# Kernel tuning notes

Hardware: AMD Instinct MI355X
Metric: run time of the kernel (lower is better)

## Reference

```python
import jax, jax.numpy as jnp
import numpy as np

TAYLOR_ORDER = 16      # Taylor terms after scaling (||A_s|| <= 0.5 -> machine precision)
MAX_SQUARINGS = 16     # fixed upper bound on squaring steps (jit-friendly)


def batched_expm(A):
    """Vectorized scaling-and-squaring matrix exponential for A of shape [..., n, n].

    Replaces the original per-item torch.linalg.matrix_exp Python loop with one
    fused batched computation (same math: exp(Q*t)).
    """
    n = A.shape[-1]
    I = jnp.eye(n, dtype=A.dtype)
    # per-matrix infinity norm [...,]
    nrm = jnp.max(jnp.sum(jnp.abs(A), axis=-1), axis=-1)
    # number of squarings so that scaled norm <= 0.5
    s = jnp.clip(jnp.ceil(jnp.log2(jnp.maximum(nrm, 1e-30) / 0.5)), 0.0, float(MAX_SQUARINGS))
    As = A * jnp.exp2(-s)[..., None, None]
    # Taylor series: P = I + As + As^2/2! + ...
    P = jnp.broadcast_to(I, A.shape)
    term = P
    for k in range(1, TAYLOR_ORDER + 1):
        term = jnp.matmul(term, As) / k
        P = P + term
    # undo scaling: square s times (data-dependent count via masked squaring)
    s_b = s[..., None, None]
    for i in range(MAX_SQUARINGS):
        P = jnp.where(s_b > i, jnp.matmul(P, P), P)
    return P


def setup_inputs() -> dict:
    key = jax.random.key(0)
    k1, k2 = jax.random.split(key)
    rate_matrix = jax.random.normal(k1, (64, 32768, 4, 4), dtype=jnp.float32)
    time = jax.random.uniform(k2, (64,), dtype=jnp.float32)
    return {"rate_matrix": rate_matrix, "time": time}


def reference(rate_matrix, time):
    # Qt = rate_matrix[i, j] * time[i], batched over (batch, seq_len)
    Qt = rate_matrix * time[:, None, None, None]
    return batched_expm(Qt)  # [B, S, 4, 4] transition probability matrices
```

## Files before the change

kernel.cpp:

```cpp
#include <hip/hip_runtime.h>
#include <math.h>


constexpr int TAYLOR_N = 10;

__global__ void __launch_bounds__(256) expm4_kernel(
    const float* __restrict__ A,
    const float* __restrict__ tvec,
    float* __restrict__ out,
    int M, int S)
{
    const int m = blockIdx.x * 256 + threadIdx.x;
    if (m >= M) return;

    const float t = tvec[m / S];

    float a[16];
    const float4* Ap = reinterpret_cast<const float4*>(A) + (size_t)m * 4;
    #pragma unroll
    for (int i = 0; i < 4; ++i) {
        float4 v = Ap[i];
        a[4*i+0] = v.x * t;
        a[4*i+1] = v.y * t;
        a[4*i+2] = v.z * t;
        a[4*i+3] = v.w * t;
    }

    float nrm = 0.0f;
    #pragma unroll
    for (int i = 0; i < 4; ++i) {
        float rs = fabsf(a[4*i+0]) + fabsf(a[4*i+1])
                 + fabsf(a[4*i+2]) + fabsf(a[4*i+3]);
        nrm = fmaxf(nrm, rs);
    }

    float sf = ceilf(log2f(fmaxf(nrm, 1e-30f) * 2.0f));
    sf = fminf(fmaxf(sf, 0.0f), 16.0f);
    const int   si    = (int)sf;
    const float scale = exp2f(-sf);
    #pragma unroll
    for (int i = 0; i < 16; ++i) a[i] *= scale;

    float P[16], T[16];
    #pragma unroll
    for (int i = 0; i < 16; ++i) { T[i] = a[i]; P[i] = a[i]; }
    P[0] += 1.0f; P[5] += 1.0f; P[10] += 1.0f; P[15] += 1.0f;

    #pragma unroll
    for (int k = 2; k <= TAYLOR_N; ++k) {
        const float rk = 1.0f / (float)k;
        #pragma unroll
        for (int i = 0; i < 4; ++i) {
            const float t0 = T[4*i+0], t1 = T[4*i+1];
            const float t2 = T[4*i+2], t3 = T[4*i+3];
            #pragma unroll
            for (int j = 0; j < 4; ++j) {
                float v = t0*a[j] + t1*a[4+j] + t2*a[8+j] + t3*a[12+j];
                v *= rk;
                T[4*i+j] = v;
                P[4*i+j] += v;
            }
        }
    }

    for (int it = 0; it < si; ++it) {
        float Q[16];
        #pragma unroll
        for (int i = 0; i < 4; ++i) {
            const float p0 = P[4*i+0], p1 = P[4*i+1];
            const float p2 = P[4*i+2], p3 = P[4*i+3];
            #pragma unroll
            for (int j = 0; j < 4; ++j) {
                Q[4*i+j] = p0*P[j] + p1*P[4+j] + p2*P[8+j] + p3*P[12+j];
            }
        }
        #pragma unroll
        for (int i = 0; i < 16; ++i) P[i] = Q[i];
    }

    float4* Op = reinterpret_cast<float4*>(out) + (size_t)m * 4;
    #pragma unroll
    for (int i = 0; i < 4; ++i) {
        float4 v;
        v.x = P[4*i+0]; v.y = P[4*i+1]; v.z = P[4*i+2]; v.w = P[4*i+3];
        Op[i] = v;
    }
}

extern "C" void kernel_launch(void* const* d_in, const int* in_sizes, int n_in,
                              void* d_out, int out_size, void* d_ws, size_t ws_size,
                              hipStream_t stream) {
    const float* A    = (const float*)d_in[0];
    const float* tvec = (const float*)d_in[1];
    float* out        = (float*)d_out;

    const int B = in_sizes[1];
    const int M = in_sizes[0] / 16;
    const int S = M / B;

    const int threads = 256;
    const int blocks  = (M + threads - 1) / threads;
    expm4_kernel<<<blocks, threads, 0, stream>>>(A, tvec, out, M, S);
}
```

Baseline: 231.9 us.

## Rewrite expm kernel with Paterson-Stockmeyer, packed math, and prefetching grid-stride loop

Replaces the sequential degree-10 Taylor evaluation with a Paterson-Stockmeyer style scheme built from A^2 and A^3, using packed float2 FMAs. The log2/exp2 scaling is replaced by exponent bit manipulation. The kernel becomes a grid-stride loop that double-buffers input loads through inline-asm global loads with manual waitcnt, and writes results with inline-asm stores. The time index per block is precomputed to avoid integer division. Together these aim to cut ALU work and hide memory latency, at the cost of fragile inline asm and reliance on the exact shape divisibility.

```diff
diff --git a/kernel.cpp b/kernel.cpp
--- a/kernel.cpp
+++ b/kernel.cpp
@@ -2,89 +2,206 @@
 #include <math.h>
 
 
-constexpr int TAYLOR_N = 10;
-
-__global__ void __launch_bounds__(256) expm4_kernel(
+typedef float f4 __attribute__((ext_vector_type(4)));
+typedef float f2 __attribute__((ext_vector_type(2)));
+
+constexpr int TPB   = 256;
+constexpr int KITER = 8;
+
+#define PREF(r, ptr)                                                         \
+    asm volatile("global_load_dwordx4 %0, %4, off\n\t"                       \
+                 "global_load_dwordx4 %1, %4, off offset:16\n\t"             \
+                 "global_load_dwordx4 %2, %4, off offset:32\n\t"             \
+                 "global_load_dwordx4 %3, %4, off offset:48"                 \
+                 : "=&v"(r##0), "=&v"(r##1), "=&v"(r##2), "=&v"(r##3)        \
+                 : "v"((const void*)(ptr)))
+
+#define WAITBUF(r)                                                           \
+    asm volatile("s_waitcnt vmcnt(4)"                                        \
+                 : "+v"(r##0), "+v"(r##1), "+v"(r##2), "+v"(r##3))
+
+#define STORE4(ptr, o0, o1, o2, o3)                                          \
+    asm volatile("global_store_dwordx4 %0, %1, off\n\t"                      \
+                 "global_store_dwordx4 %0, %2, off offset:16\n\t"            \
+                 "global_store_dwordx4 %0, %3, off offset:32\n\t"            \
+                 "global_store_dwordx4 %0, %4, off offset:48"                 \
+                 :: "v"((void*)(ptr)), "v"(o0), "v"(o1), "v"(o2), "v"(o3)    \
+                 : "memory")
+
+__device__ __forceinline__ f2 sp(float s) { f2 v; v.x = s; v.y = s; return v; }
+
+__device__ __forceinline__ void mm4p(f2 D[4][2], const f2 X[4][2],
+                                     const f2 Y[4][2])
+{
+    #pragma unroll
+    for (int i = 0; i < 4; ++i) {
+        const float x0 = X[i][0].x, x1 = X[i][0].y;
+        const float x2 = X[i][1].x, x3 = X[i][1].y;
+        #pragma unroll
+        for (int p = 0; p < 2; ++p) {
+            f2 acc = sp(x0) * Y[0][p];
+            acc = sp(x1) * Y[1][p] + acc;
+            acc = sp(x2) * Y[2][p] + acc;
+            acc = sp(x3) * Y[3][p] + acc;
+            D[i][p] = acc;
+        }
+    }
+}
+
+__device__ __forceinline__ void expm4_one(f4 r0, f4 r1, f4 r2, f4 r3, float t,
+                                          f4& o0, f4& o1, f4& o2, f4& o3)
+{
+    float nrm = fmaxf(
+        fmaxf(fabsf(r0.x)+fabsf(r0.y)+fabsf(r0.z)+fabsf(r0.w),
+              fabsf(r1.x)+fabsf(r1.y)+fabsf(r1.z)+fabsf(r1.w)),
+        fmaxf(fabsf(r2.x)+fabsf(r2.y)+fabsf(r2.z)+fabsf(r2.w),
+              fabsf(r3.x)+fabsf(r3.y)+fabsf(r3.z)+fabsf(r3.w)));
+    nrm *= fabsf(t);
+
+    const float    x = fmaxf(nrm, 1e-30f) * 2.0f;
+    const unsigned u = __float_as_uint(x);
+    int si = (int)(u >> 23) - 127 + ((u & 0x7fffffu) != 0u);
+    si = si < 0 ? 0 : (si > 16 ? 16 : si);
+    const float c = t * __uint_as_float((unsigned)(127 - si) << 23);
+
+    const f2 cc = sp(c);
+    f2 a[4][2];
+    a[0][0] = r0.xy * cc;  a[0][1] = r0.zw * cc;
+    a[1][0] = r1.xy * cc;  a[1][1] = r1.zw * cc;
+    a[2][0] = r2.xy * cc;  a[2][1] = r2.zw * cc;
+    a[3][0] = r3.xy * cc;  a[3][1] = r3.zw * cc;
+
+    f2 A2[4][2], A3[4][2];
+    mm4p(A2, a, a);
+    mm4p(A3, A2, a);
+
+    constexpr float C2 = 1.0f/2.0f,     C3 = 1.0f/6.0f;
+    constexpr float C4 = 1.0f/24.0f,    C5 = 1.0f/120.0f;
+    constexpr float C6 = 1.0f/720.0f,   C7 = 1.0f/5040.0f;
+    constexpr float C8 = 1.0f/40320.0f, C9 = 1.0f/362880.0f;
+
+    f2 G[4][2], HI[4][2], PI[4][2];
+    #pragma unroll
+    for (int i = 0; i < 4; ++i) {
+        #pragma unroll
+        for (int p = 0; p < 2; ++p) {
+            G[i][p]  = sp(C9) * A3[i][p] + (sp(C8) * A2[i][p] + sp(C7) * a[i][p]);
+            HI[i][p] = sp(C5) * A2[i][p] + sp(C4) * a[i][p];
+            PI[i][p] = sp(C2) * A2[i][p] + a[i][p];
+        }
+    }
+    G[0][0].x  += C6;   G[1][0].y  += C6;   G[2][1].x  += C6;   G[3][1].y  += C6;
+    HI[0][0].x += C3;   HI[1][0].y += C3;   HI[2][1].x += C3;   HI[3][1].y += C3;
+    PI[0][0].x += 1.0f; PI[1][0].y += 1.0f; PI[2][1].x += 1.0f; PI[3][1].y += 1.0f;
+
+    f2 H[4][2];
+    #pragma unroll
+    for (int i = 0; i < 4; ++i) {
+        const float g0 = G[i][0].x, g1 = G[i][0].y;
+        const float g2 = G[i][1].x, g3 = G[i][1].y;
+        #pragma unroll
+        for (int p = 0; p < 2; ++p) {
+            f2 v = HI[i][p];
+            v = sp(g0) * A3[0][p] + v;
+            v = sp(g1) * A3[1][p] + v;
+            v = sp(g2) * A3[2][p] + v;
+            v = sp(g3) * A3[3][p] + v;
+            H[i][p] = v;
+        }
+    }
+
+    f2 P[4][2];
+    #pragma unroll
+    for (int i = 0; i < 4; ++i) {
+        const float h0 = H[i][0].x, h1 = H[i][0].y;
+        const float h2 = H[i][1].x, h3 = H[i][1].y;
+        #pragma unroll
+        for (int p = 0; p < 2; ++p) {
+            f2 v = PI[i][p];
+            v = sp(h0) * A3[0][p] + v;
+            v = sp(h1) * A3[1][p] + v;
+            v = sp(h2) * A3[2][p] + v;
+            v = sp(h3) * A3[3][p] + v;
+            P[i][p] = v;
+        }
+    }
+
+    int it = si;
+    while (it >= 2) {
+        f2 Q[4][2];
+        mm4p(Q, P, P);
+        mm4p(P, Q, Q);
+        it -= 2;
+    }
+    if (it) {
+        f2 Q[4][2];
+        mm4p(Q, P, P);
+        #pragma unroll
+        for (int i = 0; i < 4; ++i) { P[i][0] = Q[i][0]; P[i][1] = Q[i][1]; }
+    }
+
+    o0.x = P[0][0].x; o0.y = P[0][0].y; o0.z = P[0][1].x; o0.w = P[0][1].y;
+    o1.x = P[1][0].x; o1.y = P[1][0].y; o1.z = P[1][1].x; o1.w = P[1][1].y;
+    o2.x = P[2][0].x; o2.y = P[2][0].y; o2.z = P[2][1].x; o2.w = P[2][1].y;
+    o3.x = P[3][0].x; o3.y = P[3][0].y; o3.z = P[3][1].x; o3.w = P[3][1].y;
+}
+
+__global__ void __launch_bounds__(TPB, 4) expm4_kernel(
     const float* __restrict__ A,
     const float* __restrict__ tvec,
     float* __restrict__ out,
-    int M, int S)
+    int M, int S, int sdivb, int tinc)
 {
-    const int m = blockIdx.x * 256 + threadIdx.x;
-    if (m >= M) return;
-
-    const float t = tvec[m / S];
-
-    float a[16];
-    const float4* Ap = reinterpret_cast<const float4*>(A) + (size_t)m * 4;
-    #pragma unroll
-    for (int i = 0; i < 4; ++i) {
-        float4 v = Ap[i];
-        a[4*i+0] = v.x * t;
-        a[4*i+1] = v.y * t;
-        a[4*i+2] = v.z * t;
-        a[4*i+3] = v.w * t;
-    }
-
-    float nrm = 0.0f;
-    #pragma unroll
-    for (int i = 0; i < 4; ++i) {
-        float rs = fabsf(a[4*i+0]) + fabsf(a[4*i+1])
-                 + fabsf(a[4*i+2]) + fabsf(a[4*i+3]);
-        nrm = fmaxf(nrm, rs);
-    }
-
-    float sf = ceilf(log2f(fmaxf(nrm, 1e-30f) * 2.0f));
-    sf = fminf(fmaxf(sf, 0.0f), 16.0f);
-    const int   si    = (int)sf;
-    const float scale = exp2f(-sf);
-    #pragma unroll
-    for (int i = 0; i < 16; ++i) a[i] *= scale;
-
-    float P[16], T[16];
-    #pragma unroll
-    for (int i = 0; i < 16; ++i) { T[i] = a[i]; P[i] = a[i]; }
-    P[0] += 1.0f; P[5] += 1.0f; P[10] += 1.0f; P[15] += 1.0f;
-
-    #pragma unroll
-    for (int k = 2; k <= TAYLOR_N; ++k) {
-        const float rk = 1.0f / (float)k;
-        #pragma unroll
-        for (int i = 0; i < 4; ++i) {
-            const float t0 = T[4*i+0], t1 = T[4*i+1];
-            const float t2 = T[4*i+2], t3 = T[4*i+3];
-            #pragma unroll
-            for (int j = 0; j < 4; ++j) {
-                float v = t0*a[j] + t1*a[4+j] + t2*a[8+j] + t3*a[12+j];
-                v *= rk;
-                T[4*i+j] = v;
-                P[4*i+j] += v;
-            }
-        }
-    }
-
-    for (int it = 0; it < si; ++it) {
-        float Q[16];
-        #pragma unroll
-        for (int i = 0; i < 4; ++i) {
-            const float p0 = P[4*i+0], p1 = P[4*i+1];
-            const float p2 = P[4*i+2], p3 = P[4*i+3];
-            #pragma unroll
-            for (int j = 0; j < 4; ++j) {
-                Q[4*i+j] = p0*P[j] + p1*P[4+j] + p2*P[8+j] + p3*P[12+j];
-            }
-        }
-        #pragma unroll
-        for (int i = 0; i < 16; ++i) P[i] = Q[i];
-    }
-
-    float4* Op = reinterpret_cast<float4*>(out) + (size_t)m * 4;
-    #pragma unroll
-    for (int i = 0; i < 4; ++i) {
-        float4 v;
-        v.x = P[4*i+0]; v.y = P[4*i+1]; v.z = P[4*i+2]; v.w = P[4*i+3];
-        Op[i] = v;
-    }
+    const int stride = (int)gridDim.x * TPB;
+    const int m0     = (int)blockIdx.x * TPB + (int)threadIdx.x;
+    if (m0 >= M) return;
+
+    const f4* __restrict__ Ap = reinterpret_cast<const f4*>(A);
+    f4*       __restrict__ Op = reinterpret_cast<f4*>(out);
+
+    const int tbase = (sdivb > 0) ? ((int)blockIdx.x / sdivb) : 0;
+
+    f4 a0, a1, a2, a3, b0, b1, b2, b3;
+
+    int m = m0, k = 0;
+    PREF(a, Ap + (size_t)m * 4);
+    int mn = m + stride;
+
+    while (true) {
+        {
+            const float t = (tinc > 0)
+                ? tvec[tbase + k * tinc]
+                : (sdivb > 0)
+                    ? tvec[(int)(((unsigned)blockIdx.x +
+                                  (unsigned)k * gridDim.x) / (unsigned)sdivb)]
+                    : tvec[m / S];
+            const f4* pn = Ap + (size_t)(mn < M ? mn : m) * 4;
+            PREF(b, pn);
+            WAITBUF(a);
+            f4 o0, o1, o2, o3;
+            expm4_one(a0, a1, a2, a3, t, o0, o1, o2, o3);
+            STORE4(Op + (size_t)m * 4, o0, o1, o2, o3);
+            if (mn >= M) break;
+            m = mn; ++k; mn = m + stride;
+        }
+        {
+            const float t = (tinc > 0)
+                ? tvec[tbase + k * tinc]
+                : (sdivb > 0)
+                    ? tvec[(int)(((unsigned)blockIdx.x +
+                                  (unsigned)k * gridDim.x) / (unsigned)sdivb)]
+                    : tvec[m / S];
+            const f4* pn = Ap + (size_t)(mn < M ? mn : m) * 4;
+            PREF(a, pn);
+            WAITBUF(b);
+            f4 o0, o1, o2, o3;
+            expm4_one(b0, b1, b2, b3, t, o0, o1, o2, o3);
+            STORE4(Op + (size_t)m * 4, o0, o1, o2, o3);
+            if (mn >= M) break;
+            m = mn; ++k; mn = m + stride;
+        }
+    }
+    asm volatile("s_waitcnt vmcnt(0)");
 }
 
 extern "C" void kernel_launch(void* const* d_in, const int* in_sizes, int n_in,
@@ -98,7 +215,12 @@
     const int M = in_sizes[0] / 16;
     const int S = M / B;
 
-    const int threads = 256;
-    const int blocks  = (M + threads - 1) / threads;
-    expm4_kernel<<<blocks, threads, 0, stream>>>(A, tvec, out, M, S);
-}
+    const int sdivb = (S % TPB == 0) ? (S / TPB) : 0;
+
+    int blocks = (M + TPB * KITER - 1) / (TPB * KITER);
+    if (blocks < 1) blocks = 1;
+
+    const int tinc = (sdivb > 0 && blocks % sdivb == 0) ? (blocks / sdivb) : 0;
+
+    expm4_kernel<<<blocks, TPB, 0, stream>>>(A, tvec, out, M, S, sdivb, tinc);
+}
```

Measured after the change: 238.2 us. 1.03x slower.
